# Optimization experiments

Measured on AMD Instinct MI355X. Metric: run time of the kernel, lower is better.

The kernel has to match this reference:

```python
import jax, jax.numpy as jnp
import numpy as np

N_NODES = 100000
N_EDGES = 1600000
D_FEAT = 64
D_HID = 128
N_HOP = 3


def setup_inputs() -> dict:
    key = jax.random.key(0)
    ks = jax.random.split(key, 7)
    nodes = jax.random.normal(ks[0], (N_NODES, D_FEAT), dtype=jnp.float32)
    senders = jax.random.randint(ks[1], (N_EDGES,), 0, N_NODES, dtype=jnp.int32)
    receivers = jax.random.randint(ks[2], (N_EDGES,), 0, N_NODES, dtype=jnp.int32)
    # per-hop MLP params (n_hop=3 independent layers), lecun-style scaling
    W1 = jax.random.normal(ks[3], (N_HOP, D_FEAT, D_HID), dtype=jnp.float32) / np.sqrt(D_FEAT)
    b1 = jnp.zeros((N_HOP, D_HID), dtype=jnp.float32)
    W2 = jax.random.normal(ks[4], (N_HOP, D_HID, D_FEAT), dtype=jnp.float32) / np.sqrt(D_HID)
    b2 = jnp.zeros((N_HOP, D_FEAT), dtype=jnp.float32)
    return {"nodes": nodes, "senders": senders, "receivers": receivers,
            "W1": W1, "b1": b1, "W2": W2, "b2": b2}


def _gcn_hop(x, senders, receivers, w1, b1, w2, b2):
    # update_node_fn: 2-layer MLP with leaky_relu between layers
    x = jax.nn.leaky_relu(jnp.dot(x, w1) + b1)
    x = jnp.dot(x, w2) + b2
    n = x.shape[0]
    ones = jnp.ones(senders.shape, dtype=x.dtype)
    send_deg = jax.ops.segment_sum(ones, senders, num_segments=n)
    recv_deg = jax.ops.segment_sum(ones, receivers, num_segments=n)
    # symmetric normalization: D_s^{-1/2} gather -> scatter-sum -> D_r^{-1/2}
    x = x * jax.lax.rsqrt(jnp.maximum(send_deg, 1.0))[:, None]
    x = jax.ops.segment_sum(x[senders], receivers, num_segments=n)
    x = x * jax.lax.rsqrt(jnp.maximum(recv_deg, 1.0))[:, None]
    return x


def reference(nodes, senders, receivers, W1, b1, W2, b2):
    x = nodes
    for i in range(N_HOP):
        x = _gcn_hop(x, senders, receivers, W1[i], b1[i], W2[i], b2[i])
    return x
```

## Files before the change

kernel.cpp:

```cpp
#include <hip/hip_runtime.h>

#define LRELU_SLOPE 0.01f
#define NBLK_A 512
#define BIN_SZ 256
#define MAXBIN 5120
#define NC2 128

typedef unsigned short ushort_t;
typedef unsigned int uint_t;

typedef float f32x4 __attribute__((ext_vector_type(4)));
typedef short bf16x8 __attribute__((ext_vector_type(8)));
#define MFMA16(a, b, c) __builtin_amdgcn_mfma_f32_16x16x32_bf16(a, b, c, 0, 0, 0)

__device__ inline uint_t f2bf(float f) {
    unsigned u = __float_as_uint(f);
    return (u + 0x7FFFu + ((u >> 16) & 1u)) >> 16;
}

__device__ inline void split2(float v, uint_t& hi, uint_t& lo) {
    hi = f2bf(v);
    float hif = __uint_as_float(hi << 16);
    lo = f2bf(v - hif);
}

__device__ inline float4 bf4_to_f4(ushort4 v) {
    float4 r;
    r.x = __uint_as_float((unsigned)v.x << 16);
    r.y = __uint_as_float((unsigned)v.y << 16);
    r.z = __uint_as_float((unsigned)v.z << 16);
    r.w = __uint_as_float((unsigned)v.w << 16);
    return r;
}

__device__ inline void acc_bf8(uint4 v, float* a) {
    a[0] += __uint_as_float(v.x << 16);
    a[1] += __uint_as_float(v.x & 0xFFFF0000u);
    a[2] += __uint_as_float(v.y << 16);
    a[3] += __uint_as_float(v.y & 0xFFFF0000u);
    a[4] += __uint_as_float(v.z << 16);
    a[5] += __uint_as_float(v.z & 0xFFFF0000u);
    a[6] += __uint_as_float(v.w << 16);
    a[7] += __uint_as_float(v.w & 0xFFFF0000u);
}

__device__ inline void acc_bf8m(uint4 v, float ok, float* a) {
    a[0] = fmaf(__uint_as_float(v.x << 16), ok, a[0]);
    a[1] = fmaf(__uint_as_float(v.x & 0xFFFF0000u), ok, a[1]);
    a[2] = fmaf(__uint_as_float(v.y << 16), ok, a[2]);
    a[3] = fmaf(__uint_as_float(v.y & 0xFFFF0000u), ok, a[3]);
    a[4] = fmaf(__uint_as_float(v.z << 16), ok, a[4]);
    a[5] = fmaf(__uint_as_float(v.z & 0xFFFF0000u), ok, a[5]);
    a[6] = fmaf(__uint_as_float(v.w << 16), ok, a[6]);
    a[7] = fmaf(__uint_as_float(v.w & 0xFFFF0000u), ok, a[7]);
}


__global__ __launch_bounds__(256) void build1_kernel(
        const float* __restrict__ W1, const float* __restrict__ W2,
        ushort_t* __restrict__ w1p, ushort_t* __restrict__ w2p,
        const int* __restrict__ receivers, int* __restrict__ cntA, int csA,
        const int* __restrict__ senders, uint_t* __restrict__ hist, int cs2,
        int e, int nbins, int half, int nwords) {
    __shared__ uint_t lds[12544];
    int bid = blockIdx.x, t = threadIdx.x;
    if (bid < 3) {
        int hop = bid;
        const float* w1 = W1 + hop * 64 * 128;
        const float* w2 = W2 + hop * 128 * 64;
        ushort_t* p1h = w1p + (size_t)hop * 16384;
        ushort_t* p1l = p1h + 8192;
        ushort_t* p2h = w2p + (size_t)hop * 16384;
        ushort_t* p2l = p2h + 8192;
        for (int i = t; i < 8192; i += 256) {
            int j = i & 7, o = (i >> 3) & 127, cq = i >> 10;
            int k = (cq >> 2) * 32 + (cq & 3) * 8 + j;
            uint_t h, l;
            split2(w1[k * 128 + o], h, l);
            p1h[i] = (ushort_t)h; p1l[i] = (ushort_t)l;
        }
        for (int i = t; i < 8192; i += 256) {
            int j = i & 7, o = (i >> 3) & 63, cq = i >> 9;
            int k = (cq >> 2) * 32 + (cq & 3) * 8 + j;
            uint_t h, l;
            split2(w2[k * 64 + o], h, l);
            p2h[i] = (ushort_t)h; p2l[i] = (ushort_t)l;
        }
    } else if (bid < 3 + NBLK_A) {
        int* cnt = (int*)lds;
        int b = bid - 3;
        for (int i = t; i < nbins; i += 256) cnt[i] = 0;
        __syncthreads();
        int base = b * csA, lim = min(csA, e - base);
        for (int i = t; i < lim; i += 256)
            atomicAdd(&cnt[receivers[base + i] >> 8], 1);
        __syncthreads();
        for (int i = t; i < nbins; i += 256) cntA[b * nbins + i] = cnt[i];
    } else {
        int idx = bid - 3 - NBLK_A;
        int c = idx >> 1;
        int h = idx & 1;
        int hw = half >> 2;
        for (int i = t; i < hw; i += 256) lds[i] = 0;
        __syncthreads();
        int base = c * cs2, lim = min(cs2, e - base);
        int lo = h * half;
        for (int i = t; i < lim; i += 256) {
            int v = senders[base + i] - lo;
            if ((unsigned)v < (unsigned)half)
                atomicAdd(&lds[v >> 2], 1u << ((v & 3) * 8));
        }
        __syncthreads();
        uint_t* d = hist + (size_t)c * nwords + (size_t)h * hw;
        for (int i = t; i < hw; i += 256) d[i] = lds[i];
    }
}


__global__ __launch_bounds__(512) void build2_kernel(
        const int* __restrict__ cntA, int* __restrict__ offT,
        int* __restrict__ binTot, int nbins,
        const uint_t* __restrict__ hist, int* __restrict__ deg,
        int nwords, int n) {
    __shared__ int s[NBLK_A];
    int bid = blockIdx.x, t = threadIdx.x;
    if (bid < nbins) {
        int bin = bid;
        int v = cntA[t * nbins + bin];
        s[t] = v;
        __syncthreads();
        for (int off = 1; off < NBLK_A; off <<= 1) {
            int add = (t >= off) ? s[t - off] : 0;
            __syncthreads();
            s[t] += add;
            __syncthreads();
        }
        offT[bin * NBLK_A + t] = s[t] - v;
        if (t == NBLK_A - 1) binTot[bin] = s[t];
    } else {
        int w = (bid - nbins) * 512 + t;
        if (w >= nwords) return;
        uint_t run = 0;
        for (int c = 0; c < NC2; c++) run += hist[(size_t)c * nwords + w];
        int v = w * 4;
        if (v + 3 < n) {
            ((int4*)deg)[w] = make_int4(run & 255, (run >> 8) & 255,
                                        (run >> 16) & 255, (int)(run >> 24));
        } else {
            for (int j = 0; j < 4 && v + j < n; j++) deg[v + j] = (run >> (8 * j)) & 255;
        }
    }
}


__global__ __launch_bounds__(256) void binscat_kernel(const int* __restrict__ keys,
        const int* __restrict__ payload, const int* __restrict__ offT,
        const int* __restrict__ binTot,
        uint2* __restrict__ pairs, int cs, int e, int nbins) {
    __shared__ int bt[512];
    __shared__ int cur[512];
    int b = blockIdx.x, t = threadIdx.x;
    int i1 = t, i2 = t + 256;
    int o1 = (i1 < nbins) ? binTot[i1] : 0;
    int o2 = (i2 < nbins) ? binTot[i2] : 0;
    bt[i1] = o1;
    bt[i2] = o2;
    __syncthreads();
    for (int off = 1; off < nbins; off <<= 1) {
        int v1 = (i1 >= off) ? bt[i1 - off] : 0;
        int v2 = (i2 >= off) ? bt[i2 - off] : 0;
        __syncthreads();
        bt[i1] += v1;
        bt[i2] += v2;
        __syncthreads();
    }
    if (i1 < nbins) cur[i1] = (bt[i1] - o1) + offT[i1 * NBLK_A + b];
    if (i2 < nbins) cur[i2] = (bt[i2] - o2) + offT[i2 * NBLK_A + b];
    __syncthreads();
    int base = b * cs, lim = min(cs, e - base);
    for (int i = t; i < lim; i += 256) {
        int k = keys[base + i];
        int pl = payload[base + i];
        int pos = atomicAdd(&cur[k >> 8], 1);
        pairs[pos] = make_uint2((unsigned)k, (unsigned)pl);
    }
}


__global__ __launch_bounds__(256) void binsort_kernel(const uint2* __restrict__ pairs,
        const int* __restrict__ binTot, int* __restrict__ row_start,
        int* __restrict__ bucket, int nbins, int n, int e) {
    __shared__ int cnt[BIN_SZ];
    __shared__ int loc[BIN_SZ];
    __shared__ int buf[MAXBIN];
    __shared__ int e0s;
    int bin = blockIdx.x, t = threadIdx.x;
    int myv = 0;
    for (int i = t; i < bin; i += 256) myv += binTot[i];
    loc[t] = myv;
    __syncthreads();
    for (int off = 128; off > 0; off >>= 1) {
        if (t < off) loc[t] += loc[t + off];
        __syncthreads();
    }
    if (t == 0) e0s = loc[0];
    __syncthreads();
    int e0 = e0s;
    int m = binTot[bin];
    if (m > MAXBIN) m = MAXBIN;
    __syncthreads();
    cnt[t] = 0;
    __syncthreads();
    for (int i = t; i < m; i += 256)
        atomicAdd(&cnt[pairs[e0 + i].x & 255], 1);
    __syncthreads();
    int v = cnt[t];
    int node = bin * BIN_SZ + t;
    loc[t] = v;
    __syncthreads();
    for (int off = 1; off < BIN_SZ; off <<= 1) {
        int add = (t >= off) ? loc[t - off] : 0;
        __syncthreads();
        loc[t] += add;
        __syncthreads();
    }
    int excl = loc[t] - v;
    if (node < n) row_start[node] = e0 + excl;
    if (bin == nbins - 1 && t == 255) row_start[n] = e;
    cnt[t] = excl;
    __syncthreads();
    for (int i = t; i < m; i += 256) {
        uint2 pr = pairs[e0 + i];
        int pos = atomicAdd(&cnt[pr.x & 255], 1);
        buf[pos] = (int)pr.y;
    }
    __syncthreads();
    for (int i = t; i < m; i += 256) bucket[e0 + i] = buf[i];
}


template<int GATHER>
__global__ __launch_bounds__(512) void fused_mlp_kernel(const float* __restrict__ x,
        const ushort_t* __restrict__ yin, const int* __restrict__ rs,
        const int* __restrict__ bucket,
        const ushort_t* __restrict__ w1p, const float* __restrict__ b1g,
        const ushort_t* __restrict__ w2p, const float* __restrict__ b2g,
        const int* __restrict__ sdeg, ushort_t* __restrict__ y, int n) {
    __shared__ __align__(16) char smem[54272];
    ushort_t* xsh = (ushort_t*)smem;
    ushort_t* xsl = xsh + 4608;
    ushort_t* hsh = xsl + 4608;
    ushort_t* hsl = hsh + 8704;
    float* b1f   = (float*)(hsl + 8704);
    float* b2f   = b1f + 128;
    float* snorm = b2f + 64;
    float* ybuf  = (float*)smem;

    const ushort_t* w1ph = w1p;
    const ushort_t* w1pl = w1p + 8192;
    const ushort_t* w2ph = w2p;
    const ushort_t* w2pl = w2p + 8192;

    int tid = threadIdx.x;
    int nb = blockIdx.x * 64;

    if (tid < 32) ((float4*)b1f)[tid] = ((const float4*)b1g)[tid];
    else if (tid < 48) ((float4*)b2f)[tid - 32] = ((const float4*)b2g)[tid - 32];
    if (tid >= 448) {
        int t = tid - 448;
        int gn = nb + t;
        int d = (gn < n) ? sdeg[gn] : 1;
        snorm[t] = rsqrtf(fmaxf((float)d, 1.0f));
    }

    if (GATHER) {
        int node = tid >> 3, j = tid & 7;
        int gn = nb + node;
        float a[8];
        #pragma unroll
        for (int k = 0; k < 8; k++) a[k] = 0.f;
        if (gn < n) {
            int s0 = rs[gn];
            int deg = rs[gn + 1] - s0;
            const uint4* yrow = (const uint4*)yin;
            int i = 0;
            for (; i + 16 <= deg; i += 16) {
                int idx[16];
                #pragma unroll
                for (int k = 0; k < 16; k++) idx[k] = bucket[s0 + i + k];
                uint4 r0[16];
                #pragma unroll
                for (int k = 0; k < 16; k++) r0[k] = yrow[(size_t)idx[k] * 8 + j];
                #pragma unroll
                for (int k = 0; k < 16; k++) acc_bf8(r0[k], a);
            }
            for (; i < deg; i += 8) {
                int idx[8]; float ok[8];
                #pragma unroll
                for (int k = 0; k < 8; k++) {
                    int ii = i + k;
                    bool v = ii < deg;
                    idx[k] = bucket[v ? s0 + ii : s0];
                    ok[k] = v ? 1.0f : 0.0f;
                }
                uint4 rr[8];
                #pragma unroll
                for (int k = 0; k < 8; k++) rr[k] = yrow[(size_t)idx[k] * 8 + j];
                #pragma unroll
                for (int k = 0; k < 8; k++) acc_bf8m(rr[k], ok[k], a);
            }
            float sc = rsqrtf(fmaxf((float)deg, 1.0f));
            #pragma unroll
            for (int k = 0; k < 8; k++) a[k] *= sc;
        }
        uint_t h[8], l[8];
        #pragma unroll
        for (int k = 0; k < 8; k++) split2(a[k], h[k], l[k]);
        uint4 oh, ol;
        oh.x = h[0] | (h[1] << 16); oh.y = h[2] | (h[3] << 16);
        oh.z = h[4] | (h[5] << 16); oh.w = h[6] | (h[7] << 16);
        ol.x = l[0] | (l[1] << 16); ol.y = l[2] | (l[3] << 16);
        ol.z = l[4] | (l[5] << 16); ol.w = l[6] | (l[7] << 16);
        *(uint4*)&xsh[node * 72 + j * 8] = oh;
        *(uint4*)&xsl[node * 72 + j * 8] = ol;
    } else {
        for (int i = tid; i < 1024; i += 512) {
            int node = i >> 4, c4 = i & 15;
            int gn = nb + node;
            float4 v = make_float4(0.f, 0.f, 0.f, 0.f);
            if (gn < n) v = ((const float4*)x)[(size_t)gn * 16 + c4];
            uint_t h0, l0, h1, l1, h2, l2, h3, l3;
            split2(v.x, h0, l0); split2(v.y, h1, l1);
            split2(v.z, h2, l2); split2(v.w, h3, l3);
            *(uint2*)&xsh[node * 72 + c4 * 4] = make_uint2(h0 | (h1 << 16), h2 | (h3 << 16));
            *(uint2*)&xsl[node * 72 + c4 * 4] = make_uint2(l0 | (l1 << 16), l2 | (l3 << 16));
        }
    }
    __syncthreads();

    int w = tid >> 6, lane = tid & 63;
    int q = lane >> 4, m = lane & 15;
    int oq = w & 3, nh = w >> 2;
    bool even = ((m & 1) == 0);

    {
        f32x4 acc[2][2];
        #pragma unroll
        for (int a = 0; a < 2; a++)
            #pragma unroll
            for (int b = 0; b < 2; b++) acc[a][b] = (f32x4)(0.f);

        #pragma unroll
        for (int c = 0; c < 2; c++) {
            bf16x8 Ah[2], Al[2];
            #pragma unroll
            for (int nt = 0; nt < 2; nt++) {
                int node = nh * 32 + nt * 16 + m;
                Ah[nt] = *(const bf16x8*)&xsh[node * 72 + c * 32 + q * 8];
                Al[nt] = *(const bf16x8*)&xsl[node * 72 + c * 32 + q * 8];
            }
            #pragma unroll
            for (int ot = 0; ot < 2; ot++) {
                int o1 = oq * 32 + ot * 16 + m;
                size_t fo = (size_t)((c * 4 + q) * 128 + o1) * 8;
                bf16x8 Bh = *(const bf16x8*)&w1ph[fo];
                bf16x8 Bl = *(const bf16x8*)&w1pl[fo];
                #pragma unroll
                for (int nt = 0; nt < 2; nt++) {
                    acc[ot][nt] = MFMA16(Ah[nt], Bh, acc[ot][nt]);
                    acc[ot][nt] = MFMA16(Ah[nt], Bl, acc[ot][nt]);
                    acc[ot][nt] = MFMA16(Al[nt], Bh, acc[ot][nt]);
                }
            }
        }
        float b1v[2];
        b1v[0] = b1f[oq * 32 + m];
        b1v[1] = b1f[oq * 32 + 16 + m];
        #pragma unroll
        for (int ot = 0; ot < 2; ot++)
            #pragma unroll
            for (int nt = 0; nt < 2; nt++) {
                float hv[4], pv[4];
                #pragma unroll
                for (int r = 0; r < 4; r++) {
                    float t = acc[ot][nt][r] + b1v[ot];
                    hv[r] = (t > 0.f) ? t : LRELU_SLOPE * t;
                }
                #pragma unroll
                for (int r = 0; r < 4; r++) pv[r] = __shfl_xor(hv[r], 1, 64);
                int kpos = oq * 32 + ot * 16 + (m & ~1);
                #pragma unroll
                for (int rr = 0; rr < 2; rr++) {
                    int r = even ? rr : (2 + rr);
                    float vlo = even ? hv[r] : pv[r];
                    float vhi = even ? pv[r] : hv[r];
                    uint_t ah, al, bh, bl;
                    split2(vlo, ah, al);
                    split2(vhi, bh, bl);
                    int node = nh * 32 + nt * 16 + 4 * q + r;
                    *(uint_t*)&hsh[node * 136 + kpos] = ah | (bh << 16);
                    *(uint_t*)&hsl[node * 136 + kpos] = al | (bl << 16);
                }
            }
    }
    __syncthreads();

    {
        int ot2 = oq;
        f32x4 acc2[2];
        acc2[0] = (f32x4)(0.f);
        acc2[1] = (f32x4)(0.f);
        #pragma unroll
        for (int c = 0; c < 4; c++) {
            int o2 = ot2 * 16 + m;
            size_t fo = (size_t)((c * 4 + q) * 64 + o2) * 8;
            bf16x8 Bh = *(const bf16x8*)&w2ph[fo];
            bf16x8 Bl = *(const bf16x8*)&w2pl[fo];
            #pragma unroll
            for (int nt = 0; nt < 2; nt++) {
                int node = nh * 32 + nt * 16 + m;
                bf16x8 Ah = *(const bf16x8*)&hsh[node * 136 + c * 32 + q * 8];
                bf16x8 Al = *(const bf16x8*)&hsl[node * 136 + c * 32 + q * 8];
                acc2[nt] = MFMA16(Ah, Bh, acc2[nt]);
                acc2[nt] = MFMA16(Ah, Bl, acc2[nt]);
                acc2[nt] = MFMA16(Al, Bh, acc2[nt]);
            }
        }
        float b2v = b2f[ot2 * 16 + m];
        #pragma unroll
        for (int nt = 0; nt < 2; nt++)
            #pragma unroll
            for (int r = 0; r < 4; r++) {
                int node = nh * 32 + nt * 16 + 4 * q + r;
                float sn = snorm[node];
                ybuf[node * 68 + ot2 * 16 + m] = (acc2[nt][r] + b2v) * sn;
            }
    }
    __syncthreads();

    {
        int node = tid >> 3, c8 = tid & 7;
        int gn = nb + node;
        if (gn < n) {
            const float* src = &ybuf[node * 68 + c8 * 8];
            float4 v0 = *(const float4*)src;
            float4 v1 = *(const float4*)(src + 4);
            uint4 o;
            o.x = f2bf(v0.x) | (f2bf(v0.y) << 16);
            o.y = f2bf(v0.z) | (f2bf(v0.w) << 16);
            o.z = f2bf(v1.x) | (f2bf(v1.y) << 16);
            o.w = f2bf(v1.z) | (f2bf(v1.w) << 16);
            ((uint4*)y)[(size_t)gn * 8 + c8] = o;
        }
    }
}


__global__ __launch_bounds__(256) void agg_kernel(const ushort_t* __restrict__ y,
        const int* __restrict__ rs, const int* __restrict__ bucket,
        float* __restrict__ dst, int n) {
    int wid  = (blockIdx.x * 256 + threadIdx.x) >> 6;
    int lane = threadIdx.x & 63;
    int nd   = lane >> 5;
    int slot = (lane >> 4) & 1;
    int f4   = lane & 15;
    int node = wid * 2 + nd;
    if (node >= n) return;
    int s0  = rs[node];
    int deg = rs[node + 1] - s0;
    const ushort4* y4 = (const ushort4*)y;
    float4 acc = make_float4(0.f, 0.f, 0.f, 0.f);
    for (int i = slot; i < deg; i += 16) {
        int idx[8]; float ok[8];
        #pragma unroll
        for (int j = 0; j < 8; j++) {
            int ii = i + 2 * j;
            bool v = ii < deg;
            idx[j] = bucket[v ? s0 + ii : s0];
            ok[j] = v ? 1.0f : 0.0f;
        }
        #pragma unroll
        for (int j = 0; j < 8; j++) {
            float4 v4 = bf4_to_f4(y4[(size_t)idx[j] * 16 + f4]);
            acc.x = fmaf(v4.x, ok[j], acc.x);
            acc.y = fmaf(v4.y, ok[j], acc.y);
            acc.z = fmaf(v4.z, ok[j], acc.z);
            acc.w = fmaf(v4.w, ok[j], acc.w);
        }
    }
    acc.x += __shfl_xor(acc.x, 16, 64);
    acc.y += __shfl_xor(acc.y, 16, 64);
    acc.z += __shfl_xor(acc.z, 16, 64);
    acc.w += __shfl_xor(acc.w, 16, 64);
    if (slot == 0) {
        float sc = rsqrtf(fmaxf((float)deg, 1.0f));
        acc.x *= sc; acc.y *= sc; acc.z *= sc; acc.w *= sc;
        ((float4*)dst)[(size_t)node * 16 + f4] = acc;
    }
}


extern "C" void kernel_launch(void* const* d_in, const int* in_sizes, int n_in,
                              void* d_out, int out_size, void* d_ws, size_t ws_size,
                              hipStream_t stream) {
    const float* nodes     = (const float*)d_in[0];
    const int*   senders   = (const int*)d_in[1];
    const int*   receivers = (const int*)d_in[2];
    const float* W1 = (const float*)d_in[3];
    const float* b1 = (const float*)d_in[4];
    const float* W2 = (const float*)d_in[5];
    const float* b2 = (const float*)d_in[6];

    int N = in_sizes[0] / 64;
    int E = in_sizes[1];
    int NBINS = (N + BIN_SZ - 1) / BIN_SZ;
    int CSA = (E + NBLK_A - 1) / NBLK_A;
    int CS2 = (E + NC2 - 1) / NC2;
    int HALF = ((N + 7) / 8) * 4;
    int NW2 = 2 * (HALF >> 2);

    char* p = (char*)d_ws;
    auto carve = [&](size_t bytes) -> char* {
        char* r = p;
        p += (bytes + 255) & ~(size_t)255;
        return r;
    };
    ushort_t* yA   = (ushort_t*)carve((size_t)N * 64 * 2);
    ushort_t* yB   = (ushort_t*)carve((size_t)N * 64 * 2);
    int*      rs   = (int*)carve((size_t)(N + 1) * 4);
    int*      sdeg = (int*)carve((size_t)N * 4);
    int*      bucket = (int*)carve((size_t)E * 4);
    int*      binTot = (int*)carve((size_t)NBINS * 4);
    ushort_t* w1p  = (ushort_t*)carve((size_t)3 * 16384 * 2);
    ushort_t* w2p  = (ushort_t*)carve((size_t)3 * 16384 * 2);
    char* scratch  = carve((size_t)E * 8 + 2 * (size_t)NBLK_A * NBINS * 4 + 4096);
    uint2* pairs = (uint2*)scratch;
    int*   cntA  = (int*)(scratch + (size_t)E * 8);
    int*   offT  = cntA + (size_t)NBLK_A * NBINS;
    uint_t* T1   = (uint_t*)pairs;

    build1_kernel<<<3 + NBLK_A + NC2 * 2, 256, 0, stream>>>(
            W1, W2, w1p, w2p, receivers, cntA, CSA,
            senders, T1, CS2, E, NBINS, HALF, NW2);
    build2_kernel<<<NBINS + (NW2 + 511) / 512, 512, 0, stream>>>(
            cntA, offT, binTot, NBINS, T1, sdeg, NW2, N);
    binscat_kernel<<<NBLK_A, 256, 0, stream>>>(receivers, senders, offT, binTot, pairs, CSA, E, NBINS);
    binsort_kernel<<<NBINS, 256, 0, stream>>>(pairs, binTot, rs, bucket, NBINS, N, E);

    int mbf = (N + 63) / 64;
    int agg_blocks = (N / 2 + 4) / 4 + 1;

    fused_mlp_kernel<0><<<mbf, 512, 0, stream>>>(nodes, nullptr, nullptr, nullptr,
            w1p, b1, w2p, b2, sdeg, yA, N);
    fused_mlp_kernel<1><<<mbf, 512, 0, stream>>>(nullptr, yA, rs, bucket,
            w1p + 16384, b1 + 128, w2p + 16384, b2 + 64, sdeg, yB, N);
    fused_mlp_kernel<1><<<mbf, 512, 0, stream>>>(nullptr, yB, rs, bucket,
            w1p + 32768, b1 + 256, w2p + 32768, b2 + 128, sdeg, yA, N);
    agg_kernel<<<agg_blocks, 256, 0, stream>>>(yA, rs, bucket, (float*)d_out, N);
}
```

Measured before the change: 332.8 us.

## Overlap first-hop MLP with CSR bin scatter and sort in merged launches

The hop-0 MLP does not depend on the CSR build, so its blocks are split in half and appended to the bin-scatter and bin-sort kernels. Heterogeneous blocks in one grid can then run concurrently, which removes one launch and fills idle CUs while the scatter and sort run. The scatter and sort paths are converted to 512 threads with adjusted scans. In exchange, all blocks now share a 54 KB shared-memory footprint and 512-thread launch bounds, which may lower occupancy for the sort blocks.

```diff
diff --git a/kernel.cpp b/kernel.cpp
--- a/kernel.cpp
+++ b/kernel.cpp
@@ -53,6 +53,166 @@
     a[5] = fmaf(__uint_as_float(v.z & 0xFFFF0000u), ok, a[5]);
     a[6] = fmaf(__uint_as_float(v.w << 16), ok, a[6]);
     a[7] = fmaf(__uint_as_float(v.w & 0xFFFF0000u), ok, a[7]);
+}
+
+
+__device__ __forceinline__ void mlp0_body(char* smem, const float* __restrict__ x,
+        const ushort_t* __restrict__ w1p, const float* __restrict__ b1g,
+        const ushort_t* __restrict__ w2p, const float* __restrict__ b2g,
+        const int* __restrict__ sdeg, ushort_t* __restrict__ y, int n, int nb) {
+    ushort_t* xsh = (ushort_t*)smem;
+    ushort_t* xsl = xsh + 4608;
+    ushort_t* hsh = xsl + 4608;
+    ushort_t* hsl = hsh + 8704;
+    float* b1f   = (float*)(hsl + 8704);
+    float* b2f   = b1f + 128;
+    float* snorm = b2f + 64;
+    float* ybuf  = (float*)smem;
+
+    const ushort_t* w1ph = w1p;
+    const ushort_t* w1pl = w1p + 8192;
+    const ushort_t* w2ph = w2p;
+    const ushort_t* w2pl = w2p + 8192;
+
+    int tid = threadIdx.x;
+
+    if (tid < 32) ((float4*)b1f)[tid] = ((const float4*)b1g)[tid];
+    else if (tid < 48) ((float4*)b2f)[tid - 32] = ((const float4*)b2g)[tid - 32];
+    if (tid >= 448) {
+        int t = tid - 448;
+        int gn = nb + t;
+        int d = (gn < n) ? sdeg[gn] : 1;
+        snorm[t] = rsqrtf(fmaxf((float)d, 1.0f));
+    }
+
+    for (int i = tid; i < 1024; i += 512) {
+        int node = i >> 4, c4 = i & 15;
+        int gn = nb + node;
+        float4 v = make_float4(0.f, 0.f, 0.f, 0.f);
+        if (gn < n) v = ((const float4*)x)[(size_t)gn * 16 + c4];
+        uint_t h0, l0, h1, l1, h2, l2, h3, l3;
+        split2(v.x, h0, l0); split2(v.y, h1, l1);
+        split2(v.z, h2, l2); split2(v.w, h3, l3);
+        *(uint2*)&xsh[node * 72 + c4 * 4] = make_uint2(h0 | (h1 << 16), h2 | (h3 << 16));
+        *(uint2*)&xsl[node * 72 + c4 * 4] = make_uint2(l0 | (l1 << 16), l2 | (l3 << 16));
+    }
+    __syncthreads();
+
+    int w = tid >> 6, lane = tid & 63;
+    int q = lane >> 4, m = lane & 15;
+    int oq = w & 3, nh = w >> 2;
+    bool even = ((m & 1) == 0);
+
+    {
+        f32x4 acc[2][2];
+        #pragma unroll
+        for (int a = 0; a < 2; a++)
+            #pragma unroll
+            for (int b = 0; b < 2; b++) acc[a][b] = (f32x4)(0.f);
+
+        #pragma unroll
+        for (int c = 0; c < 2; c++) {
+            bf16x8 Ah[2], Al[2];
+            #pragma unroll
+            for (int nt = 0; nt < 2; nt++) {
+                int node = nh * 32 + nt * 16 + m;
+                Ah[nt] = *(const bf16x8*)&xsh[node * 72 + c * 32 + q * 8];
+                Al[nt] = *(const bf16x8*)&xsl[node * 72 + c * 32 + q * 8];
+            }
+            #pragma unroll
+            for (int ot = 0; ot < 2; ot++) {
+                int o1 = oq * 32 + ot * 16 + m;
+                size_t fo = (size_t)((c * 4 + q) * 128 + o1) * 8;
+                bf16x8 Bh = *(const bf16x8*)&w1ph[fo];
+                bf16x8 Bl = *(const bf16x8*)&w1pl[fo];
+                #pragma unroll
+                for (int nt = 0; nt < 2; nt++) {
+                    acc[ot][nt] = MFMA16(Ah[nt], Bh, acc[ot][nt]);
+                    acc[ot][nt] = MFMA16(Ah[nt], Bl, acc[ot][nt]);
+                    acc[ot][nt] = MFMA16(Al[nt], Bh, acc[ot][nt]);
+                }
+            }
+        }
+        float b1v[2];
+        b1v[0] = b1f[oq * 32 + m];
+        b1v[1] = b1f[oq * 32 + 16 + m];
+        #pragma unroll
+        for (int ot = 0; ot < 2; ot++)
+            #pragma unroll
+            for (int nt = 0; nt < 2; nt++) {
+                float hv[4], pv[4];
+                #pragma unroll
+                for (int r = 0; r < 4; r++) {
+                    float t = acc[ot][nt][r] + b1v[ot];
+                    hv[r] = (t > 0.f) ? t : LRELU_SLOPE * t;
+                }
+                #pragma unroll
+                for (int r = 0; r < 4; r++) pv[r] = __shfl_xor(hv[r], 1, 64);
+                int kpos = oq * 32 + ot * 16 + (m & ~1);
+                #pragma unroll
+                for (int rr = 0; rr < 2; rr++) {
+                    int r = even ? rr : (2 + rr);
+                    float vlo = even ? hv[r] : pv[r];
+                    float vhi = even ? pv[r] : hv[r];
+                    uint_t ah, al, bh, bl;
+                    split2(vlo, ah, al);
+                    split2(vhi, bh, bl);
+                    int node = nh * 32 + nt * 16 + 4 * q + r;
+                    *(uint_t*)&hsh[node * 136 + kpos] = ah | (bh << 16);
+                    *(uint_t*)&hsl[node * 136 + kpos] = al | (bl << 16);
+                }
+            }
+    }
+    __syncthreads();
+
+    {
+        int ot2 = oq;
+        f32x4 acc2[2];
+        acc2[0] = (f32x4)(0.f);
+        acc2[1] = (f32x4)(0.f);
+        #pragma unroll
+        for (int c = 0; c < 4; c++) {
+            int o2 = ot2 * 16 + m;
+            size_t fo = (size_t)((c * 4 + q) * 64 + o2) * 8;
+            bf16x8 Bh = *(const bf16x8*)&w2ph[fo];
+            bf16x8 Bl = *(const bf16x8*)&w2pl[fo];
+            #pragma unroll
+            for (int nt = 0; nt < 2; nt++) {
+                int node = nh * 32 + nt * 16 + m;
+                bf16x8 Ah = *(const bf16x8*)&hsh[node * 136 + c * 32 + q * 8];
+                bf16x8 Al = *(const bf16x8*)&hsl[node * 136 + c * 32 + q * 8];
+                acc2[nt] = MFMA16(Ah, Bh, acc2[nt]);
+                acc2[nt] = MFMA16(Ah, Bl, acc2[nt]);
+                acc2[nt] = MFMA16(Al, Bh, acc2[nt]);
+            }
+        }
+        float b2v = b2f[ot2 * 16 + m];
+        #pragma unroll
+        for (int nt = 0; nt < 2; nt++)
+            #pragma unroll
+            for (int r = 0; r < 4; r++) {
+                int node = nh * 32 + nt * 16 + 4 * q + r;
+                float sn = snorm[node];
+                ybuf[node * 68 + ot2 * 16 + m] = (acc2[nt][r] + b2v) * sn;
+            }
+    }
+    __syncthreads();
+
+    {
+        int node = tid >> 3, c8 = tid & 7;
+        int gn = nb + node;
+        if (gn < n) {
+            const float* src = &ybuf[node * 68 + c8 * 8];
+            float4 v0 = *(const float4*)src;
+            float4 v1 = *(const float4*)(src + 4);
+            uint4 o;
+            o.x = f2bf(v0.x) | (f2bf(v0.y) << 16);
+            o.y = f2bf(v0.z) | (f2bf(v0.w) << 16);
+            o.z = f2bf(v1.x) | (f2bf(v1.y) << 16);
+            o.w = f2bf(v1.z) | (f2bf(v1.w) << 16);
+            ((uint4*)y)[(size_t)gn * 8 + c8] = o;
+        }
+    }
 }
 
 
@@ -153,94 +313,106 @@
 }
 
 
-__global__ __launch_bounds__(256) void binscat_kernel(const int* __restrict__ keys,
-        const int* __restrict__ payload, const int* __restrict__ offT,
-        const int* __restrict__ binTot,
-        uint2* __restrict__ pairs, int cs, int e, int nbins) {
-    __shared__ int bt[512];
-    __shared__ int cur[512];
-    int b = blockIdx.x, t = threadIdx.x;
-    int i1 = t, i2 = t + 256;
-    int o1 = (i1 < nbins) ? binTot[i1] : 0;
-    int o2 = (i2 < nbins) ? binTot[i2] : 0;
-    bt[i1] = o1;
-    bt[i2] = o2;
-    __syncthreads();
-    for (int off = 1; off < nbins; off <<= 1) {
-        int v1 = (i1 >= off) ? bt[i1 - off] : 0;
-        int v2 = (i2 >= off) ? bt[i2 - off] : 0;
-        __syncthreads();
-        bt[i1] += v1;
-        bt[i2] += v2;
-        __syncthreads();
-    }
-    if (i1 < nbins) cur[i1] = (bt[i1] - o1) + offT[i1 * NBLK_A + b];
-    if (i2 < nbins) cur[i2] = (bt[i2] - o2) + offT[i2 * NBLK_A + b];
-    __syncthreads();
-    int base = b * cs, lim = min(cs, e - base);
-    for (int i = t; i < lim; i += 256) {
-        int k = keys[base + i];
-        int pl = payload[base + i];
-        int pos = atomicAdd(&cur[k >> 8], 1);
-        pairs[pos] = make_uint2((unsigned)k, (unsigned)pl);
-    }
-}
-
-
-__global__ __launch_bounds__(256) void binsort_kernel(const uint2* __restrict__ pairs,
-        const int* __restrict__ binTot, int* __restrict__ row_start,
-        int* __restrict__ bucket, int nbins, int n, int e) {
-    __shared__ int cnt[BIN_SZ];
-    __shared__ int loc[BIN_SZ];
-    __shared__ int buf[MAXBIN];
-    __shared__ int e0s;
-    int bin = blockIdx.x, t = threadIdx.x;
-    int myv = 0;
-    for (int i = t; i < bin; i += 256) myv += binTot[i];
-    loc[t] = myv;
-    __syncthreads();
-    for (int off = 128; off > 0; off >>= 1) {
-        if (t < off) loc[t] += loc[t + off];
-        __syncthreads();
-    }
-    if (t == 0) e0s = loc[0];
-    __syncthreads();
-    int e0 = e0s;
-    int m = binTot[bin];
-    if (m > MAXBIN) m = MAXBIN;
-    __syncthreads();
-    cnt[t] = 0;
-    __syncthreads();
-    for (int i = t; i < m; i += 256)
-        atomicAdd(&cnt[pairs[e0 + i].x & 255], 1);
-    __syncthreads();
-    int v = cnt[t];
-    int node = bin * BIN_SZ + t;
-    loc[t] = v;
-    __syncthreads();
-    for (int off = 1; off < BIN_SZ; off <<= 1) {
-        int add = (t >= off) ? loc[t - off] : 0;
-        __syncthreads();
-        loc[t] += add;
-        __syncthreads();
-    }
-    int excl = loc[t] - v;
-    if (node < n) row_start[node] = e0 + excl;
-    if (bin == nbins - 1 && t == 255) row_start[n] = e;
-    cnt[t] = excl;
-    __syncthreads();
-    for (int i = t; i < m; i += 256) {
-        uint2 pr = pairs[e0 + i];
-        int pos = atomicAdd(&cnt[pr.x & 255], 1);
-        buf[pos] = (int)pr.y;
-    }
-    __syncthreads();
-    for (int i = t; i < m; i += 256) bucket[e0 + i] = buf[i];
-}
-
-
-template<int GATHER>
-__global__ __launch_bounds__(512) void fused_mlp_kernel(const float* __restrict__ x,
+__global__ __launch_bounds__(512) void phase3_kernel(
+        const int* __restrict__ keys, const int* __restrict__ payload,
+        const int* __restrict__ offT, const int* __restrict__ binTot,
+        uint2* __restrict__ pairs, int cs, int e, int nbins,
+        const float* __restrict__ x,
+        const ushort_t* __restrict__ w1p, const float* __restrict__ b1g,
+        const ushort_t* __restrict__ w2p, const float* __restrict__ b2g,
+        const int* __restrict__ sdeg, ushort_t* __restrict__ y, int n) {
+    __shared__ __align__(16) char smem[54272];
+    int bid = blockIdx.x, t = threadIdx.x;
+    if (bid < NBLK_A) {
+        int* bt  = (int*)smem;
+        int* cur = bt + 512;
+        int b = bid;
+        int o1 = (t < nbins) ? binTot[t] : 0;
+        bt[t] = o1;
+        __syncthreads();
+        for (int off = 1; off < 512; off <<= 1) {
+            int add = (t >= off) ? bt[t - off] : 0;
+            __syncthreads();
+            bt[t] += add;
+            __syncthreads();
+        }
+        if (t < nbins) cur[t] = (bt[t] - o1) + offT[t * NBLK_A + b];
+        __syncthreads();
+        int base = b * cs, lim = min(cs, e - base);
+        for (int i = t; i < lim; i += 512) {
+            int k = keys[base + i];
+            int pl = payload[base + i];
+            int pos = atomicAdd(&cur[k >> 8], 1);
+            pairs[pos] = make_uint2((unsigned)k, (unsigned)pl);
+        }
+    } else {
+        mlp0_body(smem, x, w1p, b1g, w2p, b2g, sdeg, y, n, (bid - NBLK_A) * 64);
+    }
+}
+
+
+__global__ __launch_bounds__(512) void phase4_kernel(
+        const uint2* __restrict__ pairs, const int* __restrict__ binTot,
+        int* __restrict__ row_start, int* __restrict__ bucket,
+        int nbins, int e, int nA,
+        const float* __restrict__ x,
+        const ushort_t* __restrict__ w1p, const float* __restrict__ b1g,
+        const ushort_t* __restrict__ w2p, const float* __restrict__ b2g,
+        const int* __restrict__ sdeg, ushort_t* __restrict__ y, int n) {
+    __shared__ __align__(16) char smem[54272];
+    int bid = blockIdx.x, t = threadIdx.x;
+    if (bid < nbins) {
+        int* cnt = (int*)smem;
+        int* loc = cnt + 256;
+        int* buf = loc + 512;
+        int bin = bid;
+        int myv = 0;
+        for (int i = t; i < bin; i += 512) myv += binTot[i];
+        loc[t] = myv;
+        __syncthreads();
+        for (int off = 256; off > 0; off >>= 1) {
+            if (t < off) loc[t] += loc[t + off];
+            __syncthreads();
+        }
+        int e0 = loc[0];
+        int m = binTot[bin];
+        if (m > MAXBIN) m = MAXBIN;
+        __syncthreads();
+        if (t < 256) cnt[t] = 0;
+        __syncthreads();
+        for (int i = t; i < m; i += 512)
+            atomicAdd(&cnt[pairs[e0 + i].x & 255], 1);
+        __syncthreads();
+        int v = (t < 256) ? cnt[t] : 0;
+        loc[t] = v;
+        __syncthreads();
+        for (int off = 1; off < 512; off <<= 1) {
+            int add = (t >= off) ? loc[t - off] : 0;
+            __syncthreads();
+            loc[t] += add;
+            __syncthreads();
+        }
+        int excl = loc[t] - v;
+        int node = bin * BIN_SZ + t;
+        if (t < 256 && node < n) row_start[node] = e0 + excl;
+        if (bin == nbins - 1 && t == 255) row_start[n] = e;
+        __syncthreads();
+        if (t < 256) cnt[t] = excl;
+        __syncthreads();
+        for (int i = t; i < m; i += 512) {
+            uint2 pr = pairs[e0 + i];
+            int pos = atomicAdd(&cnt[pr.x & 255], 1);
+            buf[pos] = (int)pr.y;
+        }
+        __syncthreads();
+        for (int i = t; i < m; i += 512) bucket[e0 + i] = buf[i];
+    } else {
+        mlp0_body(smem, x, w1p, b1g, w2p, b2g, sdeg, y, n, (nA + bid - nbins) * 64);
+    }
+}
+
+
+__global__ __launch_bounds__(512) void fused_mlp1_kernel(
         const ushort_t* __restrict__ yin, const int* __restrict__ rs,
         const int* __restrict__ bucket,
         const ushort_t* __restrict__ w1p, const float* __restrict__ b1g,
@@ -273,7 +445,7 @@
         snorm[t] = rsqrtf(fmaxf((float)d, 1.0f));
     }
 
-    if (GATHER) {
+    {
         int node = tid >> 3, j = tid & 7;
         int gn = nb + node;
         float a[8];
@@ -323,18 +495,6 @@
         ol.z = l[4] | (l[5] << 16); ol.w = l[6] | (l[7] << 16);
         *(uint4*)&xsh[node * 72 + j * 8] = oh;
         *(uint4*)&xsl[node * 72 + j * 8] = ol;
-    } else {
-        for (int i = tid; i < 1024; i += 512) {
-            int node = i >> 4, c4 = i & 15;
-            int gn = nb + node;
-            float4 v = make_float4(0.f, 0.f, 0.f, 0.f);
-            if (gn < n) v = ((const float4*)x)[(size_t)gn * 16 + c4];
-            uint_t h0, l0, h1, l1, h2, l2, h3, l3;
-            split2(v.x, h0, l0); split2(v.y, h1, l1);
-            split2(v.z, h2, l2); split2(v.w, h3, l3);
-            *(uint2*)&xsh[node * 72 + c4 * 4] = make_uint2(h0 | (h1 << 16), h2 | (h3 << 16));
-            *(uint2*)&xsl[node * 72 + c4 * 4] = make_uint2(l0 | (l1 << 16), l2 | (l3 << 16));
-        }
     }
     __syncthreads();
 
@@ -539,22 +699,27 @@
     int*   offT  = cntA + (size_t)NBLK_A * NBINS;
     uint_t* T1   = (uint_t*)pairs;
 
+    int mbf = (N + 63) / 64;
+    int nA  = (mbf + 1) / 2;
+    int nB  = mbf - nA;
+
     build1_kernel<<<3 + NBLK_A + NC2 * 2, 256, 0, stream>>>(
             W1, W2, w1p, w2p, receivers, cntA, CSA,
             senders, T1, CS2, E, NBINS, HALF, NW2);
     build2_kernel<<<NBINS + (NW2 + 511) / 512, 512, 0, stream>>>(
             cntA, offT, binTot, NBINS, T1, sdeg, NW2, N);
-    binscat_kernel<<<NBLK_A, 256, 0, stream>>>(receivers, senders, offT, binTot, pairs, CSA, E, NBINS);
-    binsort_kernel<<<NBINS, 256, 0, stream>>>(pairs, binTot, rs, bucket, NBINS, N, E);
-
-    int mbf = (N + 63) / 64;
+    phase3_kernel<<<NBLK_A + nA, 512, 0, stream>>>(
+            receivers, senders, offT, binTot, pairs, CSA, E, NBINS,
+            nodes, w1p, b1, w2p, b2, sdeg, yA, N);
+    phase4_kernel<<<NBINS + nB, 512, 0, stream>>>(
+            pairs, binTot, rs, bucket, NBINS, E, nA,
+            nodes, w1p, b1, w2p, b2, sdeg, yA, N);
+
     int agg_blocks = (N / 2 + 4) / 4 + 1;
 
-    fused_mlp_kernel<0><<<mbf, 512, 0, stream>>>(nodes, nullptr, nullptr, nullptr,
-            w1p, b1, w2p, b2, sdeg, yA, N);
-    fused_mlp_kernel<1><<<mbf, 512, 0, stream>>>(nullptr, yA, rs, bucket,
+    fused_mlp1_kernel<<<mbf, 512, 0, stream>>>(yA, rs, bucket,
             w1p + 16384, b1 + 128, w2p + 16384, b2 + 64, sdeg, yB, N);
-    fused_mlp_kernel<1><<<mbf, 512, 0, stream>>>(nullptr, yB, rs, bucket,
+    fused_mlp1_kernel<<<mbf, 512, 0, stream>>>(yB, rs, bucket,
             w1p + 32768, b1 + 256, w2p + 32768, b2 + 128, sdeg, yA, N);
     agg_kernel<<<agg_blocks, 256, 0, stream>>>(yA, rs, bucket, (float*)d_out, N);
 }
```

Result: faster. 325.4 us (-2.2%).
